# Kernel optimization log

Measured on AMD Instinct MI355X. Metric: run time of the kernel, lower is better.

Reference implementation:

```python
import jax, jax.numpy as jnp
import numpy as np

Q_DEFAULT = 8
XI_MAX = 0.4          # center frequency of the highest-frequency wavelet (cycles/sample)
BW_RATIO = 0.8        # bandwidth-to-center-frequency ratio
LOG_EPS = 1e-6


def _make_filters(T, Q):
    """Morlet-style analytic filter bank in the Fourier domain (all static numpy)."""
    J = int(np.floor(np.log2(T / 2)))
    freqs = np.fft.fftfreq(T).astype(np.float32)          # [T], in [-0.5, 0.5)
    # first-order wavelets: J*Q filters, geometrically spaced, quality factor Q
    n1 = J * Q
    xi1 = (XI_MAX * 2.0 ** (-np.arange(n1) / Q)).astype(np.float32)
    sig1 = (BW_RATIO * xi1 / Q).astype(np.float32)
    psi1 = np.exp(-(freqs[None, :] - xi1[:, None]) ** 2 / (2.0 * sig1[:, None] ** 2)).astype(np.float32)  # [n1, T]
    # second-order wavelets: Q2 = 1, one per octave
    xi2 = (XI_MAX * 2.0 ** (-np.arange(J))).astype(np.float32)
    sig2 = (BW_RATIO * xi2).astype(np.float32)
    psi2 = np.exp(-(freqs[None, :] - xi2[:, None]) ** 2 / (2.0 * sig2[:, None] ** 2)).astype(np.float32)  # [J, T]
    # low-pass (phi): Gaussian at scale 2^J
    sigma_phi = np.float32(BW_RATIO * XI_MAX * 2.0 ** (-J))
    phi = np.exp(-(freqs ** 2) / (2.0 * sigma_phi ** 2)).astype(np.float32)  # [T]
    # valid second-order paths: xi2 strictly below xi1 (frequency-decreasing cascade)
    pair_j1, pair_k = [], []
    for k in range(J):
        for j1 in range(n1):
            if xi2[k] < xi1[j1]:
                pair_j1.append(j1)
                pair_k.append(k)
    return psi1, psi2, phi, np.asarray(pair_j1, np.int32), np.asarray(pair_k, np.int32)


def _scatter(x_flat, psi1, psi2, phi, pair_j1, pair_k):
    """x_flat: [N, T] real. Returns S: [N, 1 + n1 + n_pairs, T]."""
    xh = jnp.fft.fft(x_flat)                                   # [N, T] complex
    S0 = jnp.fft.ifft(xh * phi).real[:, None, :]               # order 0 (dropped later)
    U1 = jnp.abs(jnp.fft.ifft(xh[:, None, :] * psi1[None]))    # [N, n1, T]
    U1h = jnp.fft.fft(U1)
    S1 = jnp.fft.ifft(U1h * phi).real                          # [N, n1, T]
    U2 = jnp.abs(jnp.fft.ifft(U1h[:, pair_j1, :] * psi2[pair_k][None]))  # [N, P, T]
    S2 = jnp.fft.ifft(jnp.fft.fft(U2) * phi).real              # [N, P, T]
    return jnp.concatenate([S0, S1, S2], axis=1)


def setup_inputs() -> dict:
    key = jax.random.key(0)
    x = jax.random.normal(key, (8, 2048, 6), dtype=jnp.float32)
    return {"x": x}


def reference(x):
    B, T, C = x.shape
    psi1, psi2, phi, pj, pk = _make_filters(T, Q_DEFAULT)
    psi1, psi2, phi = jnp.asarray(psi1), jnp.asarray(psi2), jnp.asarray(phi)
    # vectorize the original per-channel Python loop: fold channels into batch
    xf = jnp.transpose(x, (0, 2, 1)).reshape(B * C, T)          # [B*C, T]
    S = _scatter(xf, psi1, psi2, phi, pj, pk)                   # [B*C, n_coef+1, T]
    out = jnp.mean(jnp.log(S[:, 1:, :] + LOG_EPS), axis=-1)     # drop order-0, log, time-mean
    return out.reshape(B, C, -1).transpose(0, 2, 1)             # [B, n_coef, C]
```

## Files before the change

kernel.cpp:

```cpp
#include <hip/hip_runtime.h>

#define NTH 256

#define PHI1 0.29504296f
#define PHI2 0.0075683594f
#define GCUT 18.0f

__device__ __forceinline__ int swz(int i) { return i ^ (((i >> 4) & 3) * 5); }

__device__ __forceinline__ float2 cmul(float2 a, float2 b) {
  return make_float2(a.x * b.x - a.y * b.y, a.x * b.y + a.y * b.x);
}

template <int W>
__device__ __forceinline__ float wsum(float v) {
#pragma unroll
  for (int off = 1; off < W; off <<= 1) v += __shfl_xor(v, off, 64);
  return v;
}

template <int M>
__device__ __forceinline__ int prevM(int i) {
  if (M == 128)
    return ((i >> 5) & 3) | (((i >> 3) & 3) << 2) | (((i >> 1) & 3) << 4) | ((i & 1) << 6);
  else if (M == 256)
    return ((i & 3) << 6) | (((i >> 2) & 3) << 4) | (((i >> 4) & 3) << 2) | ((i >> 6) & 3);
  else if (M == 512)
    return ((i >> 7) & 3) | (((i >> 5) & 3) << 2) | (((i >> 3) & 3) << 4) |
           (((i >> 1) & 3) << 6) | ((i & 1) << 8);
  else if (M == 1024)
    return ((i >> 8) & 3) | (((i >> 6) & 3) << 2) | (((i >> 4) & 3) << 4) |
           (((i >> 2) & 3) << 6) | ((i & 3) << 8);
  else
    return ((i >> 9) & 3) | (((i >> 7) & 3) << 2) | (((i >> 5) & 3) << 4) |
           (((i >> 3) & 3) << 6) | (((i >> 1) & 3) << 8) | ((i & 1) << 10);
}

template <bool INV>
__device__ __forceinline__ void dif4(float2* A, int j, int ls, float astep) {
  const int s = 1 << ls;
  const int e = j & (s - 1);
  const int base = ((j >> ls) << (ls + 2)) | e;
  float2 w1;
  __sincosf(astep * (float)e, &w1.y, &w1.x);
  if (INV) w1.y = -w1.y;
  const float2 w2 = cmul(w1, w1);
  const float2 w3 = cmul(w2, w1);
  const float2 a0 = A[swz(base)];
  const float2 a1 = A[swz(base + s)];
  const float2 a2 = A[swz(base + 2 * s)];
  const float2 a3 = A[swz(base + 3 * s)];
  const float t0x = a0.x + a2.x, t0y = a0.y + a2.y;
  const float t1x = a0.x - a2.x, t1y = a0.y - a2.y;
  const float t2x = a1.x + a3.x, t2y = a1.y + a3.y;
  const float bdx = a1.x - a3.x, bdy = a1.y - a3.y;
  const float sgn = INV ? -1.0f : 1.0f;
  const float t3x = sgn * bdy, t3y = -sgn * bdx;
  A[swz(base)]         = make_float2(t0x + t2x, t0y + t2y);
  A[swz(base + s)]     = cmul(make_float2(t1x + t3x, t1y + t3y), w1);
  A[swz(base + 2 * s)] = cmul(make_float2(t0x - t2x, t0y - t2y), w2);
  A[swz(base + 3 * s)] = cmul(make_float2(t1x - t3x, t1y - t3y), w3);
}

__device__ __forceinline__ void dit4(float2* A, int j, int ls, float astep) {
  const int s = 1 << ls;
  const int e = j & (s - 1);
  const int base = ((j >> ls) << (ls + 2)) | e;
  float2 w1;
  __sincosf(astep * (float)e, &w1.y, &w1.x);
  const float2 w2 = cmul(w1, w1);
  const float2 w3 = cmul(w2, w1);
  const float2 c0 = A[swz(base)];
  const float2 c1 = cmul(A[swz(base + s)], w1);
  const float2 c2 = cmul(A[swz(base + 2 * s)], w2);
  const float2 c3 = cmul(A[swz(base + 3 * s)], w3);
  const float t0x = c0.x + c2.x, t0y = c0.y + c2.y;
  const float t1x = c0.x - c2.x, t1y = c0.y - c2.y;
  const float t2x = c1.x + c3.x, t2y = c1.y + c3.y;
  const float bdx = c1.x - c3.x, bdy = c1.y - c3.y;
  const float t3x = bdy, t3y = -bdx;
  A[swz(base)]         = make_float2(t0x + t2x, t0y + t2y);
  A[swz(base + s)]     = make_float2(t1x + t3x, t1y + t3y);
  A[swz(base + 2 * s)] = make_float2(t0x - t2x, t0y - t2y);
  A[swz(base + 3 * s)] = make_float2(t1x - t3x, t1y - t3y);
}

__device__ __forceinline__ void r2pair(float2* A, int g) {
  const float2 a = A[swz(2 * g)];
  const float2 b = A[swz(2 * g + 1)];
  A[swz(2 * g)]     = make_float2(a.x + b.x, a.y + b.y);
  A[swz(2 * g + 1)] = make_float2(a.x - b.x, a.y - b.y);
}

template <int M> struct LMof { static constexpr int v =
  (M == 2048) ? 11 : (M == 1024) ? 10 : (M == 512) ? 9 : (M == 256) ? 8 : 7; };

template <int M, bool INV>
__device__ __forceinline__ void dif_blk(float2* A) {
  constexpr int LM = LMof<M>::v;
  constexpr int NB = M / 4;
  const int tid = (int)threadIdx.x;
#pragma unroll
  for (int ls = LM - 2; ls >= (LM & 1); ls -= 2) {
    const float astep = -1.5707963267948966f / (float)(1 << ls);
    __syncthreads();
#pragma unroll
    for (int i = 0; i < NB / NTH; ++i) dif4<INV>(A, tid + NTH * i, ls, astep);
  }
  if (LM & 1) {
    __syncthreads();
#pragma unroll
    for (int i = 0; i < (M / 2) / NTH; ++i) r2pair(A, tid + NTH * i);
  }
  __syncthreads();
}

template <int M>
__device__ __forceinline__ void dit_blk(float2* A) {
  constexpr int LM = LMof<M>::v;
  constexpr int NB = M / 4;
  const int tid = (int)threadIdx.x;
  if (LM & 1) {
    __syncthreads();
#pragma unroll
    for (int i = 0; i < (M / 2) / NTH; ++i) r2pair(A, tid + NTH * i);
  }
#pragma unroll
  for (int ls = (LM & 1); ls <= LM - 2; ls += 2) {
    const float astep = -1.5707963267948966f / (float)(1 << ls);
    __syncthreads();
#pragma unroll
    for (int i = 0; i < NB / NTH; ++i) dit4(A, tid + NTH * i, ls, astep);
  }
  __syncthreads();
}

template <int M, bool INV, int LANES>
__device__ __forceinline__ void dif_w(float2* Aw, int l) {
  constexpr int LM = LMof<M>::v;
  constexpr int NB = M / 4;
#pragma unroll
  for (int ls = LM - 2; ls >= (LM & 1); ls -= 2) {
    const float astep = -1.5707963267948966f / (float)(1 << ls);
#pragma unroll
    for (int i = 0; i < NB / LANES; ++i) dif4<INV>(Aw, l + LANES * i, ls, astep);
  }
  if (LM & 1) {
#pragma unroll
    for (int i = 0; i < (M / 2) / LANES; ++i) r2pair(Aw, l + LANES * i);
  }
}

template <int M, int LANES>
__device__ __forceinline__ void dit_w(float2* Aw, int l) {
  constexpr int LM = LMof<M>::v;
  constexpr int NB = M / 4;
  if (LM & 1) {
#pragma unroll
    for (int i = 0; i < (M / 2) / LANES; ++i) r2pair(Aw, l + LANES * i);
  }
#pragma unroll
  for (int ls = (LM & 1); ls <= LM - 2; ls += 2) {
    const float astep = -1.5707963267948966f / (float)(1 << ls);
#pragma unroll
    for (int i = 0; i < NB / LANES; ++i) dit4(Aw, l + LANES * i, ls, astep);
  }
}

__global__ __launch_bounds__(NTH) void kA(const float* __restrict__ x,
                                          float2* __restrict__ xh) {
  __shared__ float2 A[2048];
  const int n = blockIdx.x, b = n / 6, c = n % 6;
  const float* xp = x + (size_t)b * (2048 * 6) + c;
#pragma unroll
  for (int i = 0; i < 8; ++i) {
    const int t = (int)threadIdx.x + NTH * i;
    A[swz(t)] = make_float2(xp[t * 6], 0.0f);
  }
  dif_blk<2048, false>(A);
#pragma unroll
  for (int i = 0; i < 8; ++i) {
    const int t = (int)threadIdx.x + NTH * i;
    xh[(size_t)n * 2048 + prevM<2048>(t)] = A[swz(t)];
  }
}


__device__ __forceinline__ void parent_blk1024(float2* A, float* scr,
                                               const float2* __restrict__ src,
                                               float* __restrict__ out,
                                               int b, int c, int j1) {
  constexpr int M1 = 1024;
  constexpr int NR = 4;
  const int tid = (int)threadIdx.x;
  const float xi = 0.4f * exp2f(-0.125f * (float)j1);
  const float sig = 0.1f * xi;
  const float i2s = 1.0f / (2.0f * sig * sig);
#pragma unroll
  for (int i = 0; i < NR; ++i) {
    const int m = tid + NTH * i;
    float2 acc = make_float2(0.0f, 0.0f);
#pragma unroll
    for (int q = 0; q < 2; ++q) {
      const int f = m + q * M1;
      const float fr = (float)(f < 1024 ? f : f - 2048) * (1.0f / 2048.0f);
      const float d = fr - xi;
      const float dd = d * d * i2s;
      if (dd < GCUT) {
        const float g = __expf(-dd);
        const float2 v = src[f];
        acc.x += v.x * g; acc.y += v.y * g;
      }
    }
    A[swz(m)] = acc;
  }
  dif_blk<M1, true>(A);
#pragma unroll
  for (int i = 0; i < NR; ++i) {
    const int m = tid + NTH * i;
    const float2 zv = A[swz(m)];
    A[swz(m)] = make_float2(sqrtf(zv.x * zv.x + zv.y * zv.y) * (1.0f / 2048.0f), 0.0f);
  }
  dit_blk<M1>(A);
  const float invM = 1.0f / (float)M1;
  const float c0 = A[0].x * invM;
  const float2 U1 = A[1], U2 = A[2];
  const float k1 = PHI1 * 2.0f * invM, k2 = PHI2 * 2.0f * invM;
  float part = 0.0f;
#pragma unroll
  for (int i = 0; i < NR; ++i) {
    const int t = tid + NTH * i;
    float sv, cv;
    __sincosf((6.283185307179586f / (float)M1) * (float)t, &sv, &cv);
    float acc = c0 + k1 * (U1.x * cv - U1.y * sv);
    const float c2 = cv * cv - sv * sv, s2 = 2.0f * sv * cv;
    acc += k2 * (U2.x * c2 - U2.y * s2);
    part += __logf(acc + 1e-6f);
  }
  part = wsum<64>(part);
  const int lane = tid & 63, wid = tid >> 6;
  if (lane == 0) scr[wid] = part;
  __syncthreads();
  if (tid == 0)
    out[((size_t)b * 440 + j1) * 6 + c] = (scr[0] + scr[1] + scr[2] + scr[3]) * invM;
}

template <int M1>
__device__ __forceinline__ void parent_wav(float2* Aw, const float2* __restrict__ src,
                                           float* __restrict__ out,
                                           int b, int c, int j1, int l) {
  constexpr int NRW = M1 / 64;
  constexpr int F = 2048 / M1;
  const float xi = 0.4f * exp2f(-0.125f * (float)j1);
  const float sig = 0.1f * xi;
  const float i2s = 1.0f / (2.0f * sig * sig);
#pragma unroll
  for (int i = 0; i < NRW; ++i) {
    const int m = l + 64 * i;
    float2 acc = make_float2(0.0f, 0.0f);
#pragma unroll
    for (int q = 0; q < F; ++q) {
      const int f = m + q * M1;
      const float fr = (float)(f < 1024 ? f : f - 2048) * (1.0f / 2048.0f);
      const float d = fr - xi;
      const float dd = d * d * i2s;
      if (dd < GCUT) {
        const float g = __expf(-dd);
        const float2 v = src[f];
        acc.x += v.x * g; acc.y += v.y * g;
      }
    }
    Aw[swz(m)] = acc;
  }
  dif_w<M1, true, 64>(Aw, l);
#pragma unroll
  for (int i = 0; i < NRW; ++i) {
    const int m = l + 64 * i;
    const float2 zv = Aw[swz(m)];
    Aw[swz(m)] = make_float2(sqrtf(zv.x * zv.x + zv.y * zv.y) * (1.0f / 2048.0f), 0.0f);
  }
  dit_w<M1, 64>(Aw, l);
  const float invM = 1.0f / (float)M1;
  const float c0 = Aw[0].x * invM;
  const float2 U1 = Aw[1], U2 = Aw[2];
  const float k1 = PHI1 * 2.0f * invM, k2 = PHI2 * 2.0f * invM;
  float part = 0.0f;
#pragma unroll
  for (int i = 0; i < NRW; ++i) {
    const int t = l + 64 * i;
    float sv, cv;
    __sincosf((6.283185307179586f / (float)M1) * (float)t, &sv, &cv);
    float acc = c0 + k1 * (U1.x * cv - U1.y * sv);
    const float c2 = cv * cv - sv * sv, s2 = 2.0f * sv * cv;
    acc += k2 * (U2.x * c2 - U2.y * s2);
    part += __logf(acc + 1e-6f);
  }
  part = wsum<64>(part);
  if (l == 0) out[((size_t)b * 440 + j1) * 6 + c] = part * invM;
}

__device__ __forceinline__ void parent_dual(float2* Ah, const float2* __restrict__ src,
                                            float* __restrict__ out,
                                            int b, int c, int j1, int ll) {
  const float xi = 0.4f * exp2f(-0.125f * (float)j1);
  const float sig = 0.1f * xi;
  const float i2s = 1.0f / (2.0f * sig * sig);
#pragma unroll
  for (int i = 0; i < 4; ++i) {
    const int m = ll + 32 * i;
    float2 acc = make_float2(0.0f, 0.0f);
#pragma unroll
    for (int q = 0; q < 16; ++q) {
      const int f = m + q * 128;
      const float fr = (float)(f < 1024 ? f : f - 2048) * (1.0f / 2048.0f);
      const float d = fr - xi;
      const float dd = d * d * i2s;
      if (dd < GCUT) {
        const float g = __expf(-dd);
        const float2 v = src[f];
        acc.x += v.x * g; acc.y += v.y * g;
      }
    }
    Ah[swz(m)] = acc;
  }
  dif_w<128, true, 32>(Ah, ll);
#pragma unroll
  for (int i = 0; i < 4; ++i) {
    const int m = ll + 32 * i;
    const float2 zv = Ah[swz(m)];
    Ah[swz(m)] = make_float2(sqrtf(zv.x * zv.x + zv.y * zv.y) * (1.0f / 2048.0f), 0.0f);
  }
  dit_w<128, 32>(Ah, ll);
  const float invM = 1.0f / 128.0f;
  const float c0 = Ah[0].x * invM;
  const float2 U1 = Ah[1], U2 = Ah[2];
  const float k1 = PHI1 * 2.0f * invM, k2 = PHI2 * 2.0f * invM;
  float part = 0.0f;
#pragma unroll
  for (int i = 0; i < 4; ++i) {
    const int t = ll + 32 * i;
    float sv, cv;
    __sincosf((6.283185307179586f / 128.0f) * (float)t, &sv, &cv);
    float acc = c0 + k1 * (U1.x * cv - U1.y * sv);
    const float c2 = cv * cv - sv * sv, s2 = 2.0f * sv * cv;
    acc += k2 * (U2.x * c2 - U2.y * s2);
    part += __logf(acc + 1e-6f);
  }
  part = wsum<32>(part);
  if (ll == 0) out[((size_t)b * 440 + j1) * 6 + c] = part * invM;
}

template <int M2>
__device__ __forceinline__ void desc_wav(float2* Aw, const float2* __restrict__ Vl,
                                         float* __restrict__ outp, int M1, int F,
                                         float xi, int l) {
  constexpr int NR2 = M2 / 64;
  const float sg = 0.8f * xi;
  const float i2s = 1.0f / (2.0f * sg * sg);
#pragma unroll
  for (int ii = 0; ii < NR2; ++ii) {
    const int m = l + 64 * ii;
    float2 acc = make_float2(0.0f, 0.0f);
    for (int q = 0; q < F; ++q) {
      const int f = m + q * M2;
      const float fr = (float)(f < (M1 >> 1) ? f : f - M1) * (1.0f / 2048.0f);
      const float d = fr - xi;
      const float dd = d * d * i2s;
      if (dd < GCUT) {
        const float g = __expf(-dd);
        const float2 vv = Vl[swz(f)];
        acc.x += vv.x * g; acc.y += vv.y * g;
      }
    }
    Aw[swz(m)] = acc;
  }
  dif_w<M2, true, 64>(Aw, l);
  const float invM1f = 1.0f / (float)M1;
  float b0 = 0, b1r = 0, b1i = 0, b2r = 0, b2i = 0;
#pragma unroll
  for (int ii = 0; ii < NR2; ++ii) {
    const int idx = l + 64 * ii;
    const float2 zv = Aw[swz(idx)];
    const float u = sqrtf(zv.x * zv.x + zv.y * zv.y) * invM1f;
    const int t = prevM<M2>(idx);
    float sv, cv;
    __sincosf((6.283185307179586f / (float)M2) * (float)t, &sv, &cv);
    b0 += u;
    b1r += u * cv; b1i -= u * sv;
    const float c2 = cv * cv - sv * sv, s2 = 2.0f * sv * cv;
    b2r += u * c2; b2i -= u * s2;
  }
  b0 = wsum<64>(b0);
  b1r = wsum<64>(b1r); b1i = wsum<64>(b1i);
  b2r = wsum<64>(b2r); b2i = wsum<64>(b2i);
  const float k1 = 2.0f * PHI1, k2 = 2.0f * PHI2;
  const float invM2 = 1.0f / (float)M2;
  float part = 0.0f;
#pragma unroll
  for (int ii = 0; ii < NR2; ++ii) {
    const int idx = l + 64 * ii;
    const int t = prevM<M2>(idx);
    float sv, cv;
    __sincosf((6.283185307179586f / (float)M2) * (float)t, &sv, &cv);
    float acc = b0 + k1 * (b1r * cv - b1i * sv);
    const float c2 = cv * cv - sv * sv, s2 = 2.0f * sv * cv;
    acc += k2 * (b2r * c2 - b2i * s2);
    part += __logf(acc * invM2 + 1e-6f);
  }
  part = wsum<64>(part);
  if (l == 0) *outp = part * invM2;
}

__device__ __forceinline__ void desc_dual(float2* Ah, const float2* __restrict__ Vl,
                                          float* __restrict__ outp, int M1, int F,
                                          float xi, int ll) {
  const float sg = 0.8f * xi;
  const float i2s = 1.0f / (2.0f * sg * sg);
#pragma unroll
  for (int ii = 0; ii < 4; ++ii) {
    const int m = ll + 32 * ii;
    float2 acc = make_float2(0.0f, 0.0f);
    for (int q = 0; q < F; ++q) {
      const int f = m + q * 128;
      const float fr = (float)(f < (M1 >> 1) ? f : f - M1) * (1.0f / 2048.0f);
      const float d = fr - xi;
      const float dd = d * d * i2s;
      if (dd < GCUT) {
        const float g = __expf(-dd);
        const float2 vv = Vl[swz(f)];
        acc.x += vv.x * g; acc.y += vv.y * g;
      }
    }
    Ah[swz(m)] = acc;
  }
  dif_w<128, true, 32>(Ah, ll);
  const float invM1f = 1.0f / (float)M1;
  float b0 = 0, b1r = 0, b1i = 0, b2r = 0, b2i = 0;
#pragma unroll
  for (int ii = 0; ii < 4; ++ii) {
    const int idx = ll + 32 * ii;
    const float2 zv = Ah[swz(idx)];
    const float u = sqrtf(zv.x * zv.x + zv.y * zv.y) * invM1f;
    const int t = prevM<128>(idx);
    float sv, cv;
    __sincosf((6.283185307179586f / 128.0f) * (float)t, &sv, &cv);
    b0 += u;
    b1r += u * cv; b1i -= u * sv;
    const float c2 = cv * cv - sv * sv, s2 = 2.0f * sv * cv;
    b2r += u * c2; b2i -= u * s2;
  }
  b0 = wsum<32>(b0);
  b1r = wsum<32>(b1r); b1i = wsum<32>(b1i);
  b2r = wsum<32>(b2r); b2i = wsum<32>(b2i);
  const float k1 = 2.0f * PHI1, k2 = 2.0f * PHI2;
  const float invM2 = 1.0f / 128.0f;
  float part = 0.0f;
#pragma unroll
  for (int ii = 0; ii < 4; ++ii) {
    const int idx = ll + 32 * ii;
    const int t = prevM<128>(idx);
    float sv, cv;
    __sincosf((6.283185307179586f / 128.0f) * (float)t, &sv, &cv);
    float acc = b0 + k1 * (b1r * cv - b1i * sv);
    const float c2 = cv * cv - sv * sv, s2 = 2.0f * sv * cv;
    acc += k2 * (b2r * c2 - b2i * s2);
    part += __logf(acc * invM2 + 1e-6f);
  }
  part = wsum<32>(part);
  if (ll == 0) *outp = part * invM2;
}

__device__ __forceinline__ float* o2p(float* out, int b, int c, int j1, int k) {
  return out + ((size_t)b * 440 + 80 + 4 * k * (k - 1) + j1) * 6 + c;
}
__device__ __forceinline__ float xi2f(int k) { return 0.4f * exp2f(-(float)k); }

__global__ __launch_bounds__(NTH, 4) void kBC(const float2* __restrict__ xh,
                                              float* __restrict__ out) {
  __shared__ float2 L[4096];
  const int ci = (int)blockIdx.x / 48;
  const int n  = (int)blockIdx.x % 48;
  const int b = n / 6, c = n % 6;
  const float2* src = xh + (size_t)n * 2048;
  const int tid = (int)threadIdx.x;
  const int wid = tid >> 6, l = tid & 63;
  const int h = l >> 5, ll = l & 31;

  if (ci < 2) {
    const int j1 = 8 + 4 * ci + wid;
    float2* Aw = L + wid * 1024;
    float2* W  = Aw + 512;
    parent_wav<512>(Aw, src, out, b, c, j1, l);
    desc_wav<512>(W, Aw, o2p(out, b, c, j1, 2), 512, 1, xi2f(2), l);
    desc_wav<256>(W, Aw, o2p(out, b, c, j1, 3), 512, 2, xi2f(3), l);
    float2* Wh = W + h * 128;
    for (int i = 0; i < 3; ++i) {
      const int k = 4 + 2 * i + h;
      desc_dual(Wh, Aw, o2p(out, b, c, j1, k), 512, 4, xi2f(k), ll);
    }
  } else if (ci < 4) {
    const int j1 = 16 + 4 * (ci - 2) + wid;
    float2* Aw = L + wid * 512;
    float2* W  = Aw + 256;
    parent_wav<256>(Aw, src, out, b, c, j1, l);
    desc_wav<256>(W, Aw, o2p(out, b, c, j1, 3), 256, 1, xi2f(3), l);
    float2* Wh = W + h * 128;
    for (int i = 0; i < 3; ++i) {
      const int k = 4 + 2 * i + h;
      desc_dual(Wh, Aw, o2p(out, b, c, j1, k), 256, 2, xi2f(k), ll);
    }
  } else if (ci < 12) {
    const int j1 = ci - 4;
    float* scr = (float*)(L + 3968);
    parent_blk1024(L, scr, src, out, b, c, j1);
    if (wid == 0) {
      desc_wav<1024>(L + 1024, L, o2p(out, b, c, j1, 1), 1024, 1, xi2f(1), l);
    } else if (wid == 1) {
      desc_wav<512>(L + 2048, L, o2p(out, b, c, j1, 2), 1024, 2, xi2f(2), l);
      const int k = 5 + h;
      desc_dual(L + 3328 + h * 128, L, o2p(out, b, c, j1, k), 1024, 8, xi2f(k), ll);
    } else if (wid == 2) {
      desc_wav<512>(L + 2560, L, o2p(out, b, c, j1, 3), 1024, 2, xi2f(3), l);
      const int k = 7 + h;
      desc_dual(L + 3584 + h * 128, L, o2p(out, b, c, j1, k), 1024, 8, xi2f(k), ll);
    } else {
      desc_wav<256>(L + 3072, L, o2p(out, b, c, j1, 4), 1024, 4, xi2f(4), l);
      if (h == 0)
        desc_dual(L + 3840, L, o2p(out, b, c, j1, 9), 1024, 8, xi2f(9), ll);
    }
  } else {
    const int o = ci - 9;
    const int j1 = 8 * o + 2 * wid + h;
    float2* Ah = L + (2 * wid + h) * 256;
    parent_dual(Ah, src, out, b, c, j1, ll);
    float2* W = Ah + 128;
    for (int k = o + 1; k <= 9; ++k)
      desc_dual(W, Ah, o2p(out, b, c, j1, k), 128, 1, xi2f(k), ll);
  }
}

extern "C" void kernel_launch(void* const* d_in, const int* in_sizes, int n_in,
                              void* d_out, int out_size, void* d_ws, size_t ws_size,
                              hipStream_t stream) {
  (void)in_sizes; (void)n_in; (void)out_size; (void)ws_size;
  const float* x = (const float*)d_in[0];
  float* out = (float*)d_out;
  float2* xh = (float2*)d_ws;
  kA<<<dim3(48), dim3(NTH), 0, stream>>>(x, xh);
  kBC<<<dim3(19 * 48), dim3(NTH), 0, stream>>>(xh, out);
}
```

Baseline: 85.74 us.

## Rebalance scattering blocks by splitting descendant filters across half-wavefronts

Measured after the change: 128.8 us. 50.2% more time.

```diff
diff --git a/kernel.cpp b/kernel.cpp
--- a/kernel.cpp
+++ b/kernel.cpp
@@ -411,17 +411,19 @@
   if (l == 0) *outp = part * invM2;
 }
 
-__device__ __forceinline__ void desc_dual(float2* Ah, const float2* __restrict__ Vl,
+template <int M2>
+__device__ __forceinline__ void desc_half(float2* Ah, const float2* __restrict__ Vl,
                                           float* __restrict__ outp, int M1, int F,
                                           float xi, int ll) {
+  constexpr int NR2 = M2 / 32;
   const float sg = 0.8f * xi;
   const float i2s = 1.0f / (2.0f * sg * sg);
 #pragma unroll
-  for (int ii = 0; ii < 4; ++ii) {
+  for (int ii = 0; ii < NR2; ++ii) {
     const int m = ll + 32 * ii;
     float2 acc = make_float2(0.0f, 0.0f);
     for (int q = 0; q < F; ++q) {
-      const int f = m + q * 128;
+      const int f = m + q * M2;
       const float fr = (float)(f < (M1 >> 1) ? f : f - M1) * (1.0f / 2048.0f);
       const float d = fr - xi;
       const float dd = d * d * i2s;
@@ -433,17 +435,17 @@
     }
     Ah[swz(m)] = acc;
   }
-  dif_w<128, true, 32>(Ah, ll);
+  dif_w<M2, true, 32>(Ah, ll);
   const float invM1f = 1.0f / (float)M1;
   float b0 = 0, b1r = 0, b1i = 0, b2r = 0, b2i = 0;
 #pragma unroll
-  for (int ii = 0; ii < 4; ++ii) {
+  for (int ii = 0; ii < NR2; ++ii) {
     const int idx = ll + 32 * ii;
     const float2 zv = Ah[swz(idx)];
     const float u = sqrtf(zv.x * zv.x + zv.y * zv.y) * invM1f;
-    const int t = prevM<128>(idx);
+    const int t = prevM<M2>(idx);
     float sv, cv;
-    __sincosf((6.283185307179586f / 128.0f) * (float)t, &sv, &cv);
+    __sincosf((6.283185307179586f / (float)M2) * (float)t, &sv, &cv);
     b0 += u;
     b1r += u * cv; b1i -= u * sv;
     const float c2 = cv * cv - sv * sv, s2 = 2.0f * sv * cv;
@@ -453,14 +455,14 @@
   b1r = wsum<32>(b1r); b1i = wsum<32>(b1i);
   b2r = wsum<32>(b2r); b2i = wsum<32>(b2i);
   const float k1 = 2.0f * PHI1, k2 = 2.0f * PHI2;
-  const float invM2 = 1.0f / 128.0f;
+  const float invM2 = 1.0f / (float)M2;
   float part = 0.0f;
 #pragma unroll
-  for (int ii = 0; ii < 4; ++ii) {
+  for (int ii = 0; ii < NR2; ++ii) {
     const int idx = ll + 32 * ii;
-    const int t = prevM<128>(idx);
+    const int t = prevM<M2>(idx);
     float sv, cv;
-    __sincosf((6.283185307179586f / 128.0f) * (float)t, &sv, &cv);
+    __sincosf((6.283185307179586f / (float)M2) * (float)t, &sv, &cv);
     float acc = b0 + k1 * (b1r * cv - b1i * sv);
     const float c2 = cv * cv - sv * sv, s2 = 2.0f * sv * cv;
     acc += k2 * (b2r * c2 - b2i * s2);
@@ -485,32 +487,10 @@
   const int tid = (int)threadIdx.x;
   const int wid = tid >> 6, l = tid & 63;
   const int h = l >> 5, ll = l & 31;
-
-  if (ci < 2) {
-    const int j1 = 8 + 4 * ci + wid;
-    float2* Aw = L + wid * 1024;
-    float2* W  = Aw + 512;
-    parent_wav<512>(Aw, src, out, b, c, j1, l);
-    desc_wav<512>(W, Aw, o2p(out, b, c, j1, 2), 512, 1, xi2f(2), l);
-    desc_wav<256>(W, Aw, o2p(out, b, c, j1, 3), 512, 2, xi2f(3), l);
-    float2* Wh = W + h * 128;
-    for (int i = 0; i < 3; ++i) {
-      const int k = 4 + 2 * i + h;
-      desc_dual(Wh, Aw, o2p(out, b, c, j1, k), 512, 4, xi2f(k), ll);
-    }
-  } else if (ci < 4) {
-    const int j1 = 16 + 4 * (ci - 2) + wid;
-    float2* Aw = L + wid * 512;
-    float2* W  = Aw + 256;
-    parent_wav<256>(Aw, src, out, b, c, j1, l);
-    desc_wav<256>(W, Aw, o2p(out, b, c, j1, 3), 256, 1, xi2f(3), l);
-    float2* Wh = W + h * 128;
-    for (int i = 0; i < 3; ++i) {
-      const int k = 4 + 2 * i + h;
-      desc_dual(Wh, Aw, o2p(out, b, c, j1, k), 256, 2, xi2f(k), ll);
-    }
-  } else if (ci < 12) {
-    const int j1 = ci - 4;
+  const int slot = 2 * wid + h;
+
+  if (ci < 8) {
+    const int j1 = ci;
     float* scr = (float*)(L + 3968);
     parent_blk1024(L, scr, src, out, b, c, j1);
     if (wid == 0) {
@@ -518,24 +498,122 @@
     } else if (wid == 1) {
       desc_wav<512>(L + 2048, L, o2p(out, b, c, j1, 2), 1024, 2, xi2f(2), l);
       const int k = 5 + h;
-      desc_dual(L + 3328 + h * 128, L, o2p(out, b, c, j1, k), 1024, 8, xi2f(k), ll);
+      desc_half<128>(L + 3328 + h * 128, L, o2p(out, b, c, j1, k), 1024, 8, xi2f(k), ll);
     } else if (wid == 2) {
       desc_wav<512>(L + 2560, L, o2p(out, b, c, j1, 3), 1024, 2, xi2f(3), l);
       const int k = 7 + h;
-      desc_dual(L + 3584 + h * 128, L, o2p(out, b, c, j1, k), 1024, 8, xi2f(k), ll);
+      desc_half<128>(L + 3584 + h * 128, L, o2p(out, b, c, j1, k), 1024, 8, xi2f(k), ll);
     } else {
       desc_wav<256>(L + 3072, L, o2p(out, b, c, j1, 4), 1024, 4, xi2f(4), l);
       if (h == 0)
-        desc_dual(L + 3840, L, o2p(out, b, c, j1, 9), 1024, 8, xi2f(9), ll);
+        desc_half<128>(L + 3840, L, o2p(out, b, c, j1, 9), 1024, 8, xi2f(9), ll);
+    }
+  } else if (ci < 12) {
+    const int g = ci - 8;
+    const int j1A = 8 + 2 * g, j1B = 9 + 2 * g;
+    if (wid == 0)      parent_wav<512>(L,       src, out, b, c, j1A, l);
+    else if (wid == 1) parent_wav<512>(L + 512, src, out, b, c, j1B, l);
+    __syncthreads();
+    const int j1 = h ? j1B : j1A;
+    const float2* V = L + h * 512;
+    if (wid == 0) {
+      float2* W = L + 1024 + h * 512;
+      desc_half<512>(W, V, o2p(out, b, c, j1, 2), 512, 1, xi2f(2), ll);
+      desc_half<128>(W, V, o2p(out, b, c, j1, 9), 512, 4, xi2f(9), ll);
+    } else if (wid == 1) {
+      float2* W = L + 2048 + h * 256;
+      desc_half<256>(W, V, o2p(out, b, c, j1, 3), 512, 2, xi2f(3), ll);
+      desc_half<128>(W, V, o2p(out, b, c, j1, 8), 512, 4, xi2f(8), ll);
+    } else if (wid == 2) {
+      float2* W = L + 2560 + h * 128;
+      desc_half<128>(W, V, o2p(out, b, c, j1, 4), 512, 4, xi2f(4), ll);
+      desc_half<128>(W, V, o2p(out, b, c, j1, 5), 512, 4, xi2f(5), ll);
+    } else {
+      float2* W = L + 2816 + h * 128;
+      desc_half<128>(W, V, o2p(out, b, c, j1, 6), 512, 4, xi2f(6), ll);
+      desc_half<128>(W, V, o2p(out, b, c, j1, 7), 512, 4, xi2f(7), ll);
+    }
+  } else if (ci < 16) {
+    const int g = ci - 12;
+    const int j1A = 16 + 2 * g, j1B = 17 + 2 * g;
+    if (wid == 0)      parent_wav<256>(L,       src, out, b, c, j1A, l);
+    else if (wid == 1) parent_wav<256>(L + 256, src, out, b, c, j1B, l);
+    __syncthreads();
+    const int j1 = h ? j1B : j1A;
+    const float2* V = L + h * 256;
+    if (wid == 0) {
+      float2* W = L + 512 + h * 256;
+      desc_half<256>(W, V, o2p(out, b, c, j1, 3), 256, 1, xi2f(3), ll);
+      desc_half<128>(W, V, o2p(out, b, c, j1, 9), 256, 2, xi2f(9), ll);
+    } else if (wid == 1) {
+      float2* W = L + 1024 + h * 128;
+      desc_half<128>(W, V, o2p(out, b, c, j1, 4), 256, 2, xi2f(4), ll);
+      desc_half<128>(W, V, o2p(out, b, c, j1, 5), 256, 2, xi2f(5), ll);
+    } else if (wid == 2) {
+      float2* W = L + 1280 + h * 128;
+      desc_half<128>(W, V, o2p(out, b, c, j1, 6), 256, 2, xi2f(6), ll);
+      desc_half<128>(W, V, o2p(out, b, c, j1, 7), 256, 2, xi2f(7), ll);
+    } else {
+      float2* W = L + 1536 + h * 128;
+      desc_half<128>(W, V, o2p(out, b, c, j1, 8), 256, 2, xi2f(8), ll);
+    }
+  } else if (ci < 22) {
+    const int oo = 3 + ((ci - 16) >> 1);
+    const int g = (ci - 16) & 1;
+    const int j1base = 8 * oo + 4 * g;
+    if (wid < 2)
+      parent_dual(L + slot * 128, src, out, b, c, j1base + slot, ll);
+    __syncthreads();
+    float2* W = L + 1024 + slot * 128;
+    if (oo == 3) {
+#pragma unroll
+      for (int i = 0; i < 3; ++i) {
+        const int t = 3 * slot + i;
+        const int p = t / 6, k = 4 + t % 6;
+        desc_half<128>(W, L + p * 128, o2p(out, b, c, j1base + p, k), 128, 1, xi2f(k), ll);
+      }
+    } else if (oo == 4) {
+#pragma unroll
+      for (int i = 0; i < 2; ++i) {
+        const int t = 2 * slot + i;
+        const int p = t / 5, k = 5 + t % 5;
+        desc_half<128>(W, L + p * 128, o2p(out, b, c, j1base + p, k), 128, 1, xi2f(k), ll);
+      }
+      if (slot < 4) {
+        const int t = 16 + slot;
+        const int p = t / 5, k = 5 + t % 5;
+        desc_half<128>(W, L + p * 128, o2p(out, b, c, j1base + p, k), 128, 1, xi2f(k), ll);
+      }
+    } else {
+#pragma unroll
+      for (int i = 0; i < 2; ++i) {
+        const int t = 2 * slot + i;
+        const int p = t >> 2, k = 6 + (t & 3);
+        desc_half<128>(W, L + p * 128, o2p(out, b, c, j1base + p, k), 128, 1, xi2f(k), ll);
+      }
     }
   } else {
-    const int o = ci - 9;
-    const int j1 = 8 * o + 2 * wid + h;
-    float2* Ah = L + (2 * wid + h) * 256;
-    parent_dual(Ah, src, out, b, c, j1, ll);
-    float2* W = Ah + 128;
-    for (int k = o + 1; k <= 9; ++k)
-      desc_dual(W, Ah, o2p(out, b, c, j1, k), 128, 1, xi2f(k), ll);
+    const int oo = ci - 16;
+    const int j1base = 8 * oo;
+    parent_dual(L + slot * 128, src, out, b, c, j1base + slot, ll);
+    __syncthreads();
+    float2* W = L + 1024 + slot * 128;
+    if (oo == 6) {
+#pragma unroll
+      for (int i = 0; i < 3; ++i) {
+        const int t = 3 * slot + i;
+        const int p = t / 3, k = 7 + t % 3;
+        desc_half<128>(W, L + p * 128, o2p(out, b, c, j1base + p, k), 128, 1, xi2f(k), ll);
+      }
+    } else if (oo == 7) {
+#pragma unroll
+      for (int i = 0; i < 2; ++i) {
+        const int k = 8 + i;
+        desc_half<128>(W, L + slot * 128, o2p(out, b, c, j1base + slot, k), 128, 1, xi2f(k), ll);
+      }
+    } else if (oo == 8) {
+      desc_half<128>(W, L + slot * 128, o2p(out, b, c, j1base + slot, 9), 128, 1, xi2f(9), ll);
+    }
   }
 }
 
@@ -547,5 +625,5 @@
   float* out = (float*)d_out;
   float2* xh = (float2*)d_ws;
   kA<<<dim3(48), dim3(NTH), 0, stream>>>(x, xh);
-  kBC<<<dim3(19 * 48), dim3(NTH), 0, stream>>>(xh, out);
-}
+  kBC<<<dim3(26 * 48), dim3(NTH), 0, stream>>>(xh, out);
+}
```
